# Optimization experiments

Measured on AMD Instinct MI355X. Metric: run time of the kernel, lower is better.

## Reference

```python
import jax, jax.numpy as jnp
import numpy as np

CLASS_NUM = 12
ROWS, COLS = 3, 4
ALPHA = 0.6

def _att_values():
    # attention_lst[i][j] = 1 / (# of 8-connected neighbors of cell i in the
    # ROWSxCOLS stimulus grid); note it is independent of j.
    i = np.arange(CLASS_NUM)
    r, c = i // COLS, i % COLS
    up, dn = (r - 1 >= 0), (r + 1 <= ROWS - 1)
    lf, rt = (c - 1 >= 0), (c + 1 <= COLS - 1)
    cnt = (up.astype(np.int32) + dn + lf + rt
           + (up & lf) + (up & rt) + (dn & lf) + (dn & rt))
    return (1.0 / cnt).astype(np.float32)

_ATT = jnp.asarray(_att_values())  # [CLASS_NUM]

def setup_inputs() -> dict:
    key = jax.random.key(0)
    k1, k2 = jax.random.split(key)
    B = 4194304
    outputs = jax.random.normal(k1, (B, CLASS_NUM), dtype=jnp.float32)
    targets = jax.random.randint(k2, (B,), 0, CLASS_NUM, dtype=jnp.int64)
    return {"outputs": outputs, "targets": targets}

def reference(outputs, targets):
    B = outputs.shape[0]
    logp = jax.nn.log_softmax(outputs, axis=1)          # [B, C]
    row_sum = jnp.sum(logp, axis=1)                     # [B]
    logp_t = jnp.take_along_axis(logp, targets[:, None], axis=1)[:, 0]  # [B]
    att = _ATT[targets]                                  # [B], row-constant label value
    # smoothed row = att everywhere, 1.0 at target =>
    # sum(logp * smoothed) = att * (row_sum - logp_t) + logp_t
    att_loss = -jnp.mean(att * (row_sum - logp_t) + logp_t)
    ce_loss = -jnp.mean(logp_t)
    return ALPHA * ce_loss + (1.0 - ALPHA) * att_loss
```

## Files before the change

### kernel.cpp

```cpp
#include <hip/hip_runtime.h>


#define CLS 12
#define ALPHA_F 0.6f
#define ROWS_PER_BLOCK 256

__device__ __constant__ float ATT_TAB[CLS] = {
    1.0f/3.0f, 1.0f/5.0f, 1.0f/5.0f, 1.0f/3.0f,
    1.0f/5.0f, 1.0f/8.0f, 1.0f/8.0f, 1.0f/5.0f,
    1.0f/3.0f, 1.0f/5.0f, 1.0f/5.0f, 1.0f/3.0f
};

__global__ __launch_bounds__(256)
void ce_ms_partial_kernel(const float* __restrict__ outputs,
                          const int*   __restrict__ targets,
                          float* __restrict__ partial,
                          int B, float inv_b)
{
    __shared__ float tile[ROWS_PER_BLOCK * CLS];
    __shared__ float warp_part[4];

    const int t = threadIdx.x;
    const int row0 = blockIdx.x * ROWS_PER_BLOCK;
    const long long f4_base = (long long)row0 * 3;
    const long long f4_total = (long long)B * 3;

    const float4* gp = reinterpret_cast<const float4*>(outputs);
    float4 v0, v1, v2;
    {
        long long g0 = f4_base + t;
        long long g1 = f4_base + t + 256;
        long long g2 = f4_base + t + 512;
        v0 = (g0 < f4_total) ? gp[g0] : make_float4(0.f, 0.f, 0.f, 0.f);
        v1 = (g1 < f4_total) ? gp[g1] : make_float4(0.f, 0.f, 0.f, 0.f);
        v2 = (g2 < f4_total) ? gp[g2] : make_float4(0.f, 0.f, 0.f, 0.f);
    }
    const int my_row = row0 + t;
    const int tgt = (my_row < B) ? targets[my_row] : 0;

    float4* tp = reinterpret_cast<float4*>(tile);
    tp[t]       = v0;
    tp[t + 256] = v1;
    tp[t + 512] = v2;
    __syncthreads();

    float acc = 0.0f;
    if (my_row < B) {
        float4 f0 = tp[t * 3 + 0];
        float4 f1 = tp[t * 3 + 1];
        float4 f2 = tp[t * 3 + 2];
        float x[CLS] = { f0.x, f0.y, f0.z, f0.w,
                         f1.x, f1.y, f1.z, f1.w,
                         f2.x, f2.y, f2.z, f2.w };

        float m = x[0];
        #pragma unroll
        for (int j = 1; j < CLS; ++j) m = fmaxf(m, x[j]);

        float se = 0.0f, rs = 0.0f;
        #pragma unroll
        for (int j = 0; j < CLS; ++j) {
            se += __expf(x[j] - m);
            rs += x[j];
        }
        float lse = m + __logf(se);

        float xt = x[0];
        #pragma unroll
        for (int j = 1; j < CLS; ++j) xt = (tgt == j) ? x[j] : xt;

        float logp_t  = xt - lse;
        float row_sum = rs - (float)CLS * lse;
        float att     = ATT_TAB[tgt];

        acc = (-ALPHA_F * logp_t
               - (1.0f - ALPHA_F) * (att * (row_sum - logp_t) + logp_t)) * inv_b;
    }

    #pragma unroll
    for (int off = 32; off > 0; off >>= 1)
        acc += __shfl_down(acc, off, 64);

    const int wave = t >> 6;
    if ((t & 63) == 0) warp_part[wave] = acc;
    __syncthreads();
    if (t == 0)
        partial[blockIdx.x] = warp_part[0] + warp_part[1] + warp_part[2] + warp_part[3];
}

__global__ __launch_bounds__(256)
void ce_ms_final_kernel(const float* __restrict__ partial, float* __restrict__ out, int n)
{
    const int t = threadIdx.x;
    float a0 = 0.f, a1 = 0.f, a2 = 0.f, a3 = 0.f;
    for (int i = t; i < n; i += 1024) {
        a0 += partial[i];
        if (i + 256 < n) a1 += partial[i + 256];
        if (i + 512 < n) a2 += partial[i + 512];
        if (i + 768 < n) a3 += partial[i + 768];
    }
    float acc = (a0 + a1) + (a2 + a3);

    #pragma unroll
    for (int off = 32; off > 0; off >>= 1)
        acc += __shfl_down(acc, off, 64);

    __shared__ float warp_part[4];
    const int wave = t >> 6;
    if ((t & 63) == 0) warp_part[wave] = acc;
    __syncthreads();
    if (t == 0)
        out[0] = warp_part[0] + warp_part[1] + warp_part[2] + warp_part[3];
}

extern "C" void kernel_launch(void* const* d_in, const int* in_sizes, int n_in,
                              void* d_out, int out_size, void* d_ws, size_t ws_size,
                              hipStream_t stream)
{
    const float* outputs = (const float*)d_in[0];
    const int*   targets = (const int*)d_in[1];
    float*       out     = (float*)d_out;
    float*       partial = (float*)d_ws;

    const int B = in_sizes[1];
    const float inv_b = 1.0f / (float)B;

    const int grid = (B + ROWS_PER_BLOCK - 1) / ROWS_PER_BLOCK;
    ce_ms_partial_kernel<<<grid, 256, 0, stream>>>(outputs, targets, partial, B, inv_b);
    ce_ms_final_kernel<<<1, 256, 0, stream>>>(partial, out, grid);
}
```

Before: 290.6 us.

## Process multiple row tiles per block with register prefetch and wave-local LDS transpose

Each block now handles eight 256-row tiles. Each wave transposes its own 64 rows through a private LDS slice, which removes the block-wide barrier. The next tile's logits and targets are prefetched into registers with nontemporal loads while the current tile is computed, and the loss is scaled once at the end. This gives fewer blocks and partials and overlaps memory with compute, at the cost of more register pressure and a separate unvectorized tail path.

```diff
diff --git a/kernel.cpp b/kernel.cpp
--- a/kernel.cpp
+++ b/kernel.cpp
@@ -3,7 +3,11 @@
 
 #define CLS 12
 #define ALPHA_F 0.6f
-#define ROWS_PER_BLOCK 256
+#define ROWS_PER_TILE 256
+#define TILES 8
+#define ROWS_PER_BLOCK (ROWS_PER_TILE * TILES)
+
+typedef float floatx4 __attribute__((ext_vector_type(4)));
 
 __device__ __constant__ float ATT_TAB[CLS] = {
     1.0f/3.0f, 1.0f/5.0f, 1.0f/5.0f, 1.0f/3.0f,
@@ -11,77 +15,100 @@
     1.0f/3.0f, 1.0f/5.0f, 1.0f/5.0f, 1.0f/3.0f
 };
 
+__device__ __forceinline__ float row_loss_compute(floatx4 f0, floatx4 f1, floatx4 f2, int t)
+{
+    float x[CLS] = { f0.x, f0.y, f0.z, f0.w,
+                     f1.x, f1.y, f1.z, f1.w,
+                     f2.x, f2.y, f2.z, f2.w };
+
+    float m = x[0];
+    #pragma unroll
+    for (int j = 1; j < CLS; ++j) m = fmaxf(m, x[j]);
+
+    float se = 0.0f, rs = 0.0f;
+    #pragma unroll
+    for (int j = 0; j < CLS; ++j) {
+        se += __expf(x[j] - m);
+        rs += x[j];
+    }
+    float lse = m + __logf(se);
+
+    float xt = x[0];
+    #pragma unroll
+    for (int j = 1; j < CLS; ++j) xt = (t == j) ? x[j] : xt;
+
+    float logp_t  = xt - lse;
+    float row_sum = rs - (float)CLS * lse;
+    float att     = ATT_TAB[t];
+
+    return -ALPHA_F * logp_t
+           - (1.0f - ALPHA_F) * (att * (row_sum - logp_t) + logp_t);
+}
+
 __global__ __launch_bounds__(256)
 void ce_ms_partial_kernel(const float* __restrict__ outputs,
                           const int*   __restrict__ targets,
                           float* __restrict__ partial,
                           int B, float inv_b)
 {
-    __shared__ float tile[ROWS_PER_BLOCK * CLS];
+    __shared__ float tile[256 * CLS];
     __shared__ float warp_part[4];
 
-    const int t = threadIdx.x;
-    const int row0 = blockIdx.x * ROWS_PER_BLOCK;
-    const long long f4_base = (long long)row0 * 3;
-    const long long f4_total = (long long)B * 3;
+    const int t    = threadIdx.x;
+    const int lane = t & 63;
+    const int wave = t >> 6;
+    floatx4* ws4 = reinterpret_cast<floatx4*>(tile) + wave * 192;
 
-    const float4* gp = reinterpret_cast<const float4*>(outputs);
-    float4 v0, v1, v2;
-    {
-        long long g0 = f4_base + t;
-        long long g1 = f4_base + t + 256;
-        long long g2 = f4_base + t + 512;
-        v0 = (g0 < f4_total) ? gp[g0] : make_float4(0.f, 0.f, 0.f, 0.f);
-        v1 = (g1 < f4_total) ? gp[g1] : make_float4(0.f, 0.f, 0.f, 0.f);
-        v2 = (g2 < f4_total) ? gp[g2] : make_float4(0.f, 0.f, 0.f, 0.f);
+    const floatx4* gp = reinterpret_cast<const floatx4*>(outputs);
+    float acc = 0.0f;
+
+    const long long blk_row0 = (long long)blockIdx.x * ROWS_PER_BLOCK;
+
+    if (blk_row0 + ROWS_PER_BLOCK <= (long long)B) {
+        const long long wrow = blk_row0 + wave * 64;
+
+        long long fb = wrow * 3;
+        floatx4 n0 = __builtin_nontemporal_load(gp + fb + lane);
+        floatx4 n1 = __builtin_nontemporal_load(gp + fb + 64 + lane);
+        floatx4 n2 = __builtin_nontemporal_load(gp + fb + 128 + lane);
+        int     nt = __builtin_nontemporal_load(targets + wrow + lane);
+
+        #pragma unroll
+        for (int k = 0; k < TILES; ++k) {
+            floatx4 c0 = n0, c1 = n1, c2 = n2;
+            int     ct = nt;
+            if (k + 1 < TILES) {
+                long long r2  = wrow + (long long)(k + 1) * ROWS_PER_TILE;
+                long long f2b = r2 * 3;
+                n0 = __builtin_nontemporal_load(gp + f2b + lane);
+                n1 = __builtin_nontemporal_load(gp + f2b + 64 + lane);
+                n2 = __builtin_nontemporal_load(gp + f2b + 128 + lane);
+                nt = __builtin_nontemporal_load(targets + r2 + lane);
+            }
+            ws4[lane]       = c0;
+            ws4[lane + 64]  = c1;
+            ws4[lane + 128] = c2;
+            floatx4 f0  = ws4[lane * 3 + 0];
+            floatx4 f1  = ws4[lane * 3 + 1];
+            floatx4 f2v = ws4[lane * 3 + 2];
+            acc += row_loss_compute(f0, f1, f2v, ct);
+        }
+    } else {
+        for (int k = 0; k < TILES; ++k) {
+            long long row = blk_row0 + (long long)k * ROWS_PER_TILE + t;
+            if (row < (long long)B) {
+                const floatx4* p = gp + row * 3;
+                acc += row_loss_compute(p[0], p[1], p[2], targets[row]);
+            }
+        }
     }
-    const int my_row = row0 + t;
-    const int tgt = (my_row < B) ? targets[my_row] : 0;
 
-    float4* tp = reinterpret_cast<float4*>(tile);
-    tp[t]       = v0;
-    tp[t + 256] = v1;
-    tp[t + 512] = v2;
-    __syncthreads();
-
-    float acc = 0.0f;
-    if (my_row < B) {
-        float4 f0 = tp[t * 3 + 0];
-        float4 f1 = tp[t * 3 + 1];
-        float4 f2 = tp[t * 3 + 2];
-        float x[CLS] = { f0.x, f0.y, f0.z, f0.w,
-                         f1.x, f1.y, f1.z, f1.w,
-                         f2.x, f2.y, f2.z, f2.w };
-
-        float m = x[0];
-        #pragma unroll
-        for (int j = 1; j < CLS; ++j) m = fmaxf(m, x[j]);
-
-        float se = 0.0f, rs = 0.0f;
-        #pragma unroll
-        for (int j = 0; j < CLS; ++j) {
-            se += __expf(x[j] - m);
-            rs += x[j];
-        }
-        float lse = m + __logf(se);
-
-        float xt = x[0];
-        #pragma unroll
-        for (int j = 1; j < CLS; ++j) xt = (tgt == j) ? x[j] : xt;
-
-        float logp_t  = xt - lse;
-        float row_sum = rs - (float)CLS * lse;
-        float att     = ATT_TAB[tgt];
-
-        acc = (-ALPHA_F * logp_t
-               - (1.0f - ALPHA_F) * (att * (row_sum - logp_t) + logp_t)) * inv_b;
-    }
+    acc *= inv_b;
 
     #pragma unroll
     for (int off = 32; off > 0; off >>= 1)
         acc += __shfl_down(acc, off, 64);
 
-    const int wave = t >> 6;
     if ((t & 63) == 0) warp_part[wave] = acc;
     __syncthreads();
     if (t == 0)
@@ -92,14 +119,9 @@
 void ce_ms_final_kernel(const float* __restrict__ partial, float* __restrict__ out, int n)
 {
     const int t = threadIdx.x;
-    float a0 = 0.f, a1 = 0.f, a2 = 0.f, a3 = 0.f;
-    for (int i = t; i < n; i += 1024) {
-        a0 += partial[i];
-        if (i + 256 < n) a1 += partial[i + 256];
-        if (i + 512 < n) a2 += partial[i + 512];
-        if (i + 768 < n) a3 += partial[i + 768];
-    }
-    float acc = (a0 + a1) + (a2 + a3);
+    float acc = 0.0f;
+    for (int i = t; i < n; i += 256)
+        acc += partial[i];
 
     #pragma unroll
     for (int off = 32; off > 0; off >>= 1)
@@ -125,7 +147,7 @@
     const int B = in_sizes[1];
     const float inv_b = 1.0f / (float)B;
 
-    const int grid = (B + ROWS_PER_BLOCK - 1) / ROWS_PER_BLOCK;
+    const int grid = (int)(((long long)B + ROWS_PER_BLOCK - 1) / ROWS_PER_BLOCK);
     ce_ms_partial_kernel<<<grid, 256, 0, stream>>>(outputs, targets, partial, B, inv_b);
     ce_ms_final_kernel<<<1, 256, 0, stream>>>(partial, out, grid);
 }
```

New measurement: 266.1 us, median of 2. 8.4% less time.
